# Kernel tuning notes

Measured on AMD Instinct MI355X. Metric: run time of the kernel, lower is better.

## Reference

```python
import jax, jax.numpy as jnp
import numpy as np
from jax import lax

C = 256
RED = 16
SK = 7  # spatial kernel


def setup_inputs() -> dict:
    key = jax.random.key(0)
    ks = jax.random.split(key, 12)
    b, c, h, w = 4, C, 64, 64
    cr = c // RED
    c8 = c // 8
    s = lambda fan_in: 1.0 / np.sqrt(fan_in)
    return {
        "x": jax.random.normal(ks[0], (b, c, h, w), dtype=jnp.float32),
        # channel MLP (nn.Linear weights are [out, in], no bias)
        "w1": jax.random.normal(ks[1], (cr, c), dtype=jnp.float32) * s(c),
        "w2": jax.random.normal(ks[2], (c, cr), dtype=jnp.float32) * s(cr),
        # spatial conv: [out=1, in=2, 7, 7], no bias
        "w_sp": jax.random.normal(ks[3], (1, 2, SK, SK), dtype=jnp.float32) * s(2 * SK * SK),
        # 1x1 convs (stored as [out, in]) with bias (Conv2d default bias=True)
        "wq": jax.random.normal(ks[4], (c8, c), dtype=jnp.float32) * s(c),
        "bq": jax.random.normal(ks[5], (c8,), dtype=jnp.float32) * s(c),
        "wk": jax.random.normal(ks[6], (c8, c), dtype=jnp.float32) * s(c),
        "bk": jax.random.normal(ks[7], (c8,), dtype=jnp.float32) * s(c),
        "wv": jax.random.normal(ks[8], (c, c), dtype=jnp.float32) * s(c),
        "bv": jax.random.normal(ks[9], (c,), dtype=jnp.float32) * s(c),
        "gamma": jnp.zeros((1,), dtype=jnp.float32),
    }


def reference(x, w1, w2, w_sp, wq, bq, wk, bk, wv, bv, gamma):
    b, c, h, w = x.shape
    hw = h * w

    # ---- channel attention (CBAM) ----
    avg = jnp.mean(x, axis=(2, 3))          # [b, c]
    mx = jnp.max(x, axis=(2, 3))            # [b, c]
    mlp = lambda v: jax.nn.relu(v @ w1.T) @ w2.T
    ch_att = jax.nn.sigmoid(mlp(avg) + mlp(mx))[:, :, None, None]
    x = x * ch_att

    # ---- spatial attention (CBAM) ----
    avg_s = jnp.mean(x, axis=1, keepdims=True)
    max_s = jnp.max(x, axis=1, keepdims=True)
    sp_in = jnp.concatenate([avg_s, max_s], axis=1)  # [b, 2, h, w]
    pad = SK // 2
    sp = lax.conv_general_dilated(
        sp_in, w_sp, window_strides=(1, 1), padding=[(pad, pad), (pad, pad)],
        dimension_numbers=("NCHW", "OIHW", "NCHW"))
    x = x * jax.nn.sigmoid(sp)

    # ---- non-local self-attention (single head, unscaled) ----
    q = jnp.einsum("bchw,oc->bohw", x, wq) + bq[None, :, None, None]
    k = jnp.einsum("bchw,oc->bohw", x, wk) + bk[None, :, None, None]
    v = jnp.einsum("bchw,oc->bohw", x, wv) + bv[None, :, None, None]
    q = q.reshape(b, -1, hw).transpose(0, 2, 1)   # [b, hw, c/8]
    k = k.reshape(b, -1, hw)                      # [b, c/8, hw]
    v = v.reshape(b, c, hw)                       # [b, c, hw]

    attn = jax.nn.softmax(jnp.einsum("bid,bdj->bij", q, k), axis=-1)  # [b, hw, hw]
    out = jnp.einsum("bcj,bij->bci", v, attn).reshape(b, c, h, w)

    return gamma[0] * out + x
```

## Files before the change

kernel.cpp:

```cpp
#include <hip/hip_runtime.h>
#include <math.h>

constexpr int B_  = 4;
constexpr int C_  = 256;
constexpr int HW_ = 4096;
constexpr int CR_ = 16;
constexpr int CQ_ = 32;

__device__ __forceinline__ float sigmoidf_(float x){ return 1.f/(1.f+expf(-x)); }

__device__ __forceinline__ void ch_att_inline(
    int b, int t,
    const float* __restrict__ avg, const float* __restrict__ mxv,
    const float* __restrict__ w1,  const float* __restrict__ w2,
    float* sa, float* sm, float* pa, float* pm, float* hs, float* satt){
  sa[t] = avg[b*C_+t]; sm[t] = mxv[b*C_+t];
  __syncthreads();
  int h = t >> 4, seg = t & 15;
  float qa = 0.f, qm = 0.f;
  #pragma unroll
  for (int c2 = 0; c2 < 16; c2++){
    int c = seg*16 + c2;
    float w = w1[h*C_ + c];
    qa += w*sa[c]; qm += w*sm[c];
  }
  pa[t] = qa; pm[t] = qm;
  __syncthreads();
  if (t < CR_){
    float ha = 0.f, hm = 0.f;
    #pragma unroll
    for (int s = 0; s < 16; s++){ ha += pa[t*16+s]; hm += pm[t*16+s]; }
    hs[t] = fmaxf(ha, 0.f) + fmaxf(hm, 0.f);
  }
  __syncthreads();
  float o = 0.f;
  #pragma unroll
  for (int h2 = 0; h2 < CR_; h2++) o += hs[h2]*w2[t*CR_+h2];
  satt[t] = sigmoidf_(o);
  __syncthreads();
}

__global__ void kA(const float* __restrict__ x, float* __restrict__ avg, float* __restrict__ mxv){
  int bc = blockIdx.x;
  const float4* r4 = (const float4*)(x + (size_t)bc*HW_);
  float s = 0.f, m = -INFINITY;
  for (int i = threadIdx.x; i < HW_/4; i += 256){
    float4 v = r4[i];
    s += v.x+v.y+v.z+v.w;
    m = fmaxf(m, fmaxf(fmaxf(v.x,v.y), fmaxf(v.z,v.w)));
  }
  for (int off = 32; off; off >>= 1){
    s += __shfl_down(s, off);
    m = fmaxf(m, __shfl_down(m, off));
  }
  __shared__ float ss[4], sm[4];
  int w = threadIdx.x >> 6, lane = threadIdx.x & 63;
  if (!lane){ ss[w] = s; sm[w] = m; }
  __syncthreads();
  if (!threadIdx.x){
    avg[bc] = (ss[0]+ss[1]+ss[2]+ss[3]) * (1.f/HW_);
    mxv[bc] = fmaxf(fmaxf(sm[0],sm[1]), fmaxf(sm[2],sm[3]));
  }
}

__global__ void kBC(const float* __restrict__ x,
                    const float* __restrict__ avg, const float* __restrict__ mxv,
                    const float* __restrict__ w1,  const float* __restrict__ w2,
                    float* __restrict__ avgs, float* __restrict__ maxs){
  int b = blockIdx.x >> 6, r = blockIdx.x & 63, t = threadIdx.x;
  __shared__ float sa[C_], sm[C_], pa[C_], pm[C_], hs[CR_], satt[C_];
  __shared__ float4 rs[16][16], rm[16][16];
  ch_att_inline(b, t, avg, mxv, w1, w2, sa, sm, pa, pm, hs, satt);

  int cg = t >> 4, q = t & 15;
  const float4* x4 = (const float4*)x;
  float4 s = {0.f,0.f,0.f,0.f};
  float4 m = {-INFINITY,-INFINITY,-INFINITY,-INFINITY};
  #pragma unroll
  for (int j = 0; j < 16; j++){
    int c = cg*16 + j;
    float a = satt[c];
    float4 v = x4[(size_t)(b*C_+c)*(HW_/4) + (r<<4) + q];
    float vx=v.x*a, vy=v.y*a, vz=v.z*a, vw=v.w*a;
    s.x+=vx; s.y+=vy; s.z+=vz; s.w+=vw;
    m.x=fmaxf(m.x,vx); m.y=fmaxf(m.y,vy); m.z=fmaxf(m.z,vz); m.w=fmaxf(m.w,vw);
  }
  rs[cg][q] = s; rm[cg][q] = m;
  __syncthreads();
  if (t < 16){
    float4 S = {0.f,0.f,0.f,0.f};
    float4 M = {-INFINITY,-INFINITY,-INFINITY,-INFINITY};
    #pragma unroll
    for (int g = 0; g < 16; g++){
      float4 a = rs[g][t], b2 = rm[g][t];
      S.x+=a.x; S.y+=a.y; S.z+=a.z; S.w+=a.w;
      M.x=fmaxf(M.x,b2.x); M.y=fmaxf(M.y,b2.y); M.z=fmaxf(M.z,b2.z); M.w=fmaxf(M.w,b2.w);
    }
    S.x*=(1.f/C_); S.y*=(1.f/C_); S.z*=(1.f/C_); S.w*=(1.f/C_);
    ((float4*)(avgs + b*HW_ + r*64))[t] = S;
    ((float4*)(maxs + b*HW_ + r*64))[t] = M;
  }
}

__global__ void kD2(const float* __restrict__ x,
                    const float* __restrict__ avg, const float* __restrict__ mxv,
                    const float* __restrict__ w1,  const float* __restrict__ w2,
                    const float* __restrict__ avgs, const float* __restrict__ maxs,
                    const float* __restrict__ wsp, float* __restrict__ out){
  int bx = blockIdx.x;
  int b = bx >> 6, rem = bx & 63, rt = rem >> 2, cp = rem & 3;
  int t = threadIdx.x;
  __shared__ float sa[C_], sm[C_], pa[C_], pm[C_], hs[CR_], satt[C_];
  __shared__ float savg[10][64], smax[10][64], ssig[4][64], swsp[98];
  if (t < 98) swsp[t] = wsp[t];
  ch_att_inline(b, t, avg, mxv, w1, w2, sa, sm, pa, pm, hs, satt);

  for (int idx = t; idx < 640; idx += 256){
    int row = idx >> 6, col = idx & 63;
    int gr = rt*4 - 3 + row;
    float s = 0.f, m = 0.f;
    if ((unsigned)gr < 64u){
      s = avgs[b*HW_ + gr*64 + col];
      m = maxs[b*HW_ + gr*64 + col];
    }
    savg[row][col] = s; smax[row][col] = m;
  }
  __syncthreads();
  int trow = t >> 6, col = t & 63;
  float acc = 0.f;
  #pragma unroll
  for (int ky = 0; ky < 7; ky++){
    #pragma unroll
    for (int kx = 0; kx < 7; kx++){
      int gx = col - 3 + kx;
      if ((unsigned)gx < 64u)
        acc += savg[trow+ky][gx]*swsp[ky*7+kx] + smax[trow+ky][gx]*swsp[49+ky*7+kx];
    }
  }
  ssig[trow][col] = sigmoidf_(acc);
  __syncthreads();
  int f4id = t & 63;
  float4 sg4 = ((const float4*)ssig)[f4id];
  int imgo = rt*64 + f4id;
  const float4* x4 = (const float4*)x;
  float4* o4 = (float4*)out;
  #pragma unroll
  for (int jj = 0; jj < 16; jj++){
    int lc = (t>>6) + jj*4;
    float a = satt[cp*64 + lc];
    size_t g = (size_t)(b*C_ + cp*64 + lc)*(HW_/4) + imgo;
    float4 v = x4[g];
    float4 rr;
    rr.x = v.x*a*sg4.x; rr.y = v.y*a*sg4.y; rr.z = v.z*a*sg4.z; rr.w = v.w*a*sg4.w;
    o4[g] = rr;
  }
}

__global__ void kE(const float* __restrict__ gamma, const float* __restrict__ x3,
                   const float* __restrict__ wq, const float* __restrict__ bq,
                   const float* __restrict__ wk, const float* __restrict__ bk,
                   const float* __restrict__ wv, const float* __restrict__ bv,
                   float* __restrict__ qb, float* __restrict__ kb, float* __restrict__ vb){
  if (gamma[0] == 0.f) return;
  int t = threadIdx.x;
  __shared__ float sx[C_*32];
  for (int bx = blockIdx.x; bx < 512; bx += gridDim.x){
    int b = bx >> 7, tile = bx & 127, p0 = tile*32;
    for (int idx = t; idx < C_*32; idx += 256){
      int c = idx >> 5, px = idx & 31;
      sx[idx] = x3[(size_t)(b*C_+c)*HW_ + p0 + px];
    }
    __syncthreads();
    for (int oi = t; oi < CQ_*32; oi += 256){
      int o = oi >> 5, px = oi & 31;
      float aq = bq[o], ak = bk[o];
      for (int c = 0; c < C_; c++){ float xv = sx[c*32+px]; aq += xv*wq[o*C_+c]; ak += xv*wk[o*C_+c]; }
      qb[(size_t)(b*CQ_+o)*HW_ + p0 + px] = aq;
      kb[(size_t)(b*CQ_+o)*HW_ + p0 + px] = ak;
    }
    for (int oi = t; oi < C_*32; oi += 256){
      int o = oi >> 5, px = oi & 31;
      float av = bv[o];
      for (int c = 0; c < C_; c++) av += sx[c*32+px]*wv[o*C_+c];
      vb[(size_t)(b*C_+o)*HW_ + p0 + px] = av;
    }
    __syncthreads();
  }
}

__global__ void kF2(const float* __restrict__ gamma, const float* __restrict__ qb,
                    const float* __restrict__ kb, const float* __restrict__ vb,
                    float* __restrict__ out){
  float g = gamma[0];
  if (g == 0.f) return;
  __shared__ float sq[CQ_];
  __shared__ float sl[HW_];
  __shared__ float red[8];
  int t = threadIdx.x;
  for (int gi = blockIdx.x; gi < B_*HW_; gi += gridDim.x){
    int b = gi >> 12, i = gi & (HW_-1);
    if (t < CQ_) sq[t] = qb[(size_t)(b*CQ_+t)*HW_ + i];
    __syncthreads();
    float lmax = -INFINITY;
    for (int j = t; j < HW_; j += 256){
      float l = 0.f;
      for (int d = 0; d < CQ_; d++) l += sq[d]*kb[(size_t)(b*CQ_+d)*HW_ + j];
      sl[j] = l; lmax = fmaxf(lmax, l);
    }
    for (int off = 32; off; off >>= 1) lmax = fmaxf(lmax, __shfl_down(lmax, off));
    if (!(t & 63)) red[t>>6] = lmax;
    __syncthreads();
    float M = fmaxf(fmaxf(red[0],red[1]), fmaxf(red[2],red[3]));
    float lsum = 0.f;
    for (int j = t; j < HW_; j += 256){ float p = expf(sl[j]-M); sl[j] = p; lsum += p; }
    for (int off = 32; off; off >>= 1) lsum += __shfl_down(lsum, off);
    if (!(t & 63)) red[4+(t>>6)] = lsum;
    __syncthreads();
    float inv = g/(red[4]+red[5]+red[6]+red[7]);
    float acc = 0.f;
    const float* vrow = vb + (size_t)(b*C_+t)*HW_;
    for (int j = 0; j < HW_; j++) acc += sl[j]*vrow[j];
    out[(size_t)(b*C_+t)*HW_ + i] += acc*inv;
    __syncthreads();
  }
}

extern "C" void kernel_launch(void* const* d_in, const int* in_sizes, int n_in,
                              void* d_out, int out_size, void* d_ws, size_t ws_size,
                              hipStream_t stream){
  const float* x   = (const float*)d_in[0];
  const float* w1  = (const float*)d_in[1];
  const float* w2  = (const float*)d_in[2];
  const float* wsp = (const float*)d_in[3];
  const float* wq  = (const float*)d_in[4];
  const float* bq  = (const float*)d_in[5];
  const float* wk  = (const float*)d_in[6];
  const float* bk  = (const float*)d_in[7];
  const float* wv  = (const float*)d_in[8];
  const float* bv  = (const float*)d_in[9];
  const float* gm  = (const float*)d_in[10];
  float* out = (float*)d_out;
  float* ws  = (float*)d_ws;

  float* avg  = ws;
  float* mxv  = avg  + B_*C_;
  float* avgs = mxv  + B_*C_;
  float* maxs = avgs + B_*HW_;
  float* qb   = maxs + B_*HW_;
  float* kb   = qb   + B_*CQ_*HW_;
  float* vb   = kb   + B_*CQ_*HW_;
  size_t need_attn = (size_t)((vb + (size_t)B_*C_*HW_) - ws) * sizeof(float);

  kA <<<B_*C_, 256, 0, stream>>>(x, avg, mxv);
  kBC<<<256,   256, 0, stream>>>(x, avg, mxv, w1, w2, avgs, maxs);
  kD2<<<256,   256, 0, stream>>>(x, avg, mxv, w1, w2, avgs, maxs, wsp, out);

  if (ws_size >= need_attn){
    kE <<<256, 256, 0, stream>>>(gm, out, wq, bq, wk, bk, wv, bv, qb, kb, vb);
    kF2<<<256, 256, 0, stream>>>(gm, qb, kb, vb, out);
  }
}
```

Measured before the change: 109.2 us.

## Fuse all stages into one persistent kernel with atomic grid barriers

Replaces the five kernel launches with one 256-block persistent kernel whose stages are separated by a software grid barrier built on an atomic counter. The channel-attention MLP is computed once per block after the first barrier instead of in two separate kernels. This removes per-launch overhead and inter-kernel gaps, but adds a memset launch and barrier spin costs, and relies on all 256 blocks being co-resident. The ws_size guard is also dropped.

```diff
diff --git a/kernel.cpp b/kernel.cpp
--- a/kernel.cpp
+++ b/kernel.cpp
@@ -6,221 +6,221 @@
 constexpr int HW_ = 4096;
 constexpr int CR_ = 16;
 constexpr int CQ_ = 32;
+constexpr int NB_ = 256;
 
 __device__ __forceinline__ float sigmoidf_(float x){ return 1.f/(1.f+expf(-x)); }
 
-__device__ __forceinline__ void ch_att_inline(
-    int b, int t,
-    const float* __restrict__ avg, const float* __restrict__ mxv,
-    const float* __restrict__ w1,  const float* __restrict__ w2,
-    float* sa, float* sm, float* pa, float* pm, float* hs, float* satt){
-  sa[t] = avg[b*C_+t]; sm[t] = mxv[b*C_+t];
+__device__ __forceinline__ void gbar(int* cnt, int gen){
   __syncthreads();
-  int h = t >> 4, seg = t & 15;
-  float qa = 0.f, qm = 0.f;
-  #pragma unroll
-  for (int c2 = 0; c2 < 16; c2++){
-    int c = seg*16 + c2;
-    float w = w1[h*C_ + c];
-    qa += w*sa[c]; qm += w*sm[c];
-  }
-  pa[t] = qa; pm[t] = qm;
-  __syncthreads();
-  if (t < CR_){
-    float ha = 0.f, hm = 0.f;
-    #pragma unroll
-    for (int s = 0; s < 16; s++){ ha += pa[t*16+s]; hm += pm[t*16+s]; }
-    hs[t] = fmaxf(ha, 0.f) + fmaxf(hm, 0.f);
-  }
-  __syncthreads();
-  float o = 0.f;
-  #pragma unroll
-  for (int h2 = 0; h2 < CR_; h2++) o += hs[h2]*w2[t*CR_+h2];
-  satt[t] = sigmoidf_(o);
+  if (threadIdx.x == 0){
+    __threadfence();
+    __hip_atomic_fetch_add(cnt, 1, __ATOMIC_RELEASE, __HIP_MEMORY_SCOPE_AGENT);
+    while (__hip_atomic_load(cnt, __ATOMIC_ACQUIRE, __HIP_MEMORY_SCOPE_AGENT) < gen*NB_)
+      __builtin_amdgcn_s_sleep(1);
+    __threadfence();
+  }
   __syncthreads();
 }
 
-__global__ void kA(const float* __restrict__ x, float* __restrict__ avg, float* __restrict__ mxv){
-  int bc = blockIdx.x;
-  const float4* r4 = (const float4*)(x + (size_t)bc*HW_);
-  float s = 0.f, m = -INFINITY;
-  for (int i = threadIdx.x; i < HW_/4; i += 256){
-    float4 v = r4[i];
-    s += v.x+v.y+v.z+v.w;
-    m = fmaxf(m, fmaxf(fmaxf(v.x,v.y), fmaxf(v.z,v.w)));
-  }
-  for (int off = 32; off; off >>= 1){
-    s += __shfl_down(s, off);
-    m = fmaxf(m, __shfl_down(m, off));
-  }
-  __shared__ float ss[4], sm[4];
-  int w = threadIdx.x >> 6, lane = threadIdx.x & 63;
-  if (!lane){ ss[w] = s; sm[w] = m; }
-  __syncthreads();
-  if (!threadIdx.x){
-    avg[bc] = (ss[0]+ss[1]+ss[2]+ss[3]) * (1.f/HW_);
-    mxv[bc] = fmaxf(fmaxf(sm[0],sm[1]), fmaxf(sm[2],sm[3]));
-  }
-}
-
-__global__ void kBC(const float* __restrict__ x,
-                    const float* __restrict__ avg, const float* __restrict__ mxv,
-                    const float* __restrict__ w1,  const float* __restrict__ w2,
-                    float* __restrict__ avgs, float* __restrict__ maxs){
-  int b = blockIdx.x >> 6, r = blockIdx.x & 63, t = threadIdx.x;
-  __shared__ float sa[C_], sm[C_], pa[C_], pm[C_], hs[CR_], satt[C_];
-  __shared__ float4 rs[16][16], rm[16][16];
-  ch_att_inline(b, t, avg, mxv, w1, w2, sa, sm, pa, pm, hs, satt);
-
-  int cg = t >> 4, q = t & 15;
-  const float4* x4 = (const float4*)x;
-  float4 s = {0.f,0.f,0.f,0.f};
-  float4 m = {-INFINITY,-INFINITY,-INFINITY,-INFINITY};
-  #pragma unroll
-  for (int j = 0; j < 16; j++){
-    int c = cg*16 + j;
-    float a = satt[c];
-    float4 v = x4[(size_t)(b*C_+c)*(HW_/4) + (r<<4) + q];
-    float vx=v.x*a, vy=v.y*a, vz=v.z*a, vw=v.w*a;
-    s.x+=vx; s.y+=vy; s.z+=vz; s.w+=vw;
-    m.x=fmaxf(m.x,vx); m.y=fmaxf(m.y,vy); m.z=fmaxf(m.z,vz); m.w=fmaxf(m.w,vw);
-  }
-  rs[cg][q] = s; rm[cg][q] = m;
-  __syncthreads();
-  if (t < 16){
-    float4 S = {0.f,0.f,0.f,0.f};
-    float4 M = {-INFINITY,-INFINITY,-INFINITY,-INFINITY};
-    #pragma unroll
-    for (int g = 0; g < 16; g++){
-      float4 a = rs[g][t], b2 = rm[g][t];
-      S.x+=a.x; S.y+=a.y; S.z+=a.z; S.w+=a.w;
-      M.x=fmaxf(M.x,b2.x); M.y=fmaxf(M.y,b2.y); M.z=fmaxf(M.z,b2.z); M.w=fmaxf(M.w,b2.w);
-    }
-    S.x*=(1.f/C_); S.y*=(1.f/C_); S.z*=(1.f/C_); S.w*=(1.f/C_);
-    ((float4*)(avgs + b*HW_ + r*64))[t] = S;
-    ((float4*)(maxs + b*HW_ + r*64))[t] = M;
-  }
-}
-
-__global__ void kD2(const float* __restrict__ x,
-                    const float* __restrict__ avg, const float* __restrict__ mxv,
-                    const float* __restrict__ w1,  const float* __restrict__ w2,
-                    const float* __restrict__ avgs, const float* __restrict__ maxs,
-                    const float* __restrict__ wsp, float* __restrict__ out){
-  int bx = blockIdx.x;
-  int b = bx >> 6, rem = bx & 63, rt = rem >> 2, cp = rem & 3;
-  int t = threadIdx.x;
-  __shared__ float sa[C_], sm[C_], pa[C_], pm[C_], hs[CR_], satt[C_];
-  __shared__ float savg[10][64], smax[10][64], ssig[4][64], swsp[98];
-  if (t < 98) swsp[t] = wsp[t];
-  ch_att_inline(b, t, avg, mxv, w1, w2, sa, sm, pa, pm, hs, satt);
-
-  for (int idx = t; idx < 640; idx += 256){
-    int row = idx >> 6, col = idx & 63;
-    int gr = rt*4 - 3 + row;
-    float s = 0.f, m = 0.f;
-    if ((unsigned)gr < 64u){
-      s = avgs[b*HW_ + gr*64 + col];
-      m = maxs[b*HW_ + gr*64 + col];
-    }
-    savg[row][col] = s; smax[row][col] = m;
-  }
-  __syncthreads();
-  int trow = t >> 6, col = t & 63;
-  float acc = 0.f;
-  #pragma unroll
-  for (int ky = 0; ky < 7; ky++){
-    #pragma unroll
-    for (int kx = 0; kx < 7; kx++){
-      int gx = col - 3 + kx;
-      if ((unsigned)gx < 64u)
-        acc += savg[trow+ky][gx]*swsp[ky*7+kx] + smax[trow+ky][gx]*swsp[49+ky*7+kx];
-    }
-  }
-  ssig[trow][col] = sigmoidf_(acc);
-  __syncthreads();
-  int f4id = t & 63;
-  float4 sg4 = ((const float4*)ssig)[f4id];
-  int imgo = rt*64 + f4id;
-  const float4* x4 = (const float4*)x;
-  float4* o4 = (float4*)out;
-  #pragma unroll
-  for (int jj = 0; jj < 16; jj++){
-    int lc = (t>>6) + jj*4;
-    float a = satt[cp*64 + lc];
-    size_t g = (size_t)(b*C_ + cp*64 + lc)*(HW_/4) + imgo;
-    float4 v = x4[g];
-    float4 rr;
-    rr.x = v.x*a*sg4.x; rr.y = v.y*a*sg4.y; rr.z = v.z*a*sg4.z; rr.w = v.w*a*sg4.w;
-    o4[g] = rr;
-  }
-}
-
-__global__ void kE(const float* __restrict__ gamma, const float* __restrict__ x3,
-                   const float* __restrict__ wq, const float* __restrict__ bq,
-                   const float* __restrict__ wk, const float* __restrict__ bk,
-                   const float* __restrict__ wv, const float* __restrict__ bv,
-                   float* __restrict__ qb, float* __restrict__ kb, float* __restrict__ vb){
-  if (gamma[0] == 0.f) return;
-  int t = threadIdx.x;
-  __shared__ float sx[C_*32];
-  for (int bx = blockIdx.x; bx < 512; bx += gridDim.x){
-    int b = bx >> 7, tile = bx & 127, p0 = tile*32;
+__global__ void __launch_bounds__(256, 1) kFused(
+    const float* __restrict__ x,
+    const float* __restrict__ w1,  const float* __restrict__ w2,
+    const float* __restrict__ wsp,
+    const float* __restrict__ wq,  const float* __restrict__ bq,
+    const float* __restrict__ wk,  const float* __restrict__ bk,
+    const float* __restrict__ wv,  const float* __restrict__ bv,
+    const float* __restrict__ gm,
+    int* cnt, float* avg, float* mxv, float* avgs, float* maxs,
+    float* qb, float* kb, float* vb, float* out){
+
+  __shared__ union {
+    struct {
+      float sa[C_], sm[C_], pa[C_], pm[C_], hs[CR_], satt[C_];
+      float4 rs[16][16], rm[16][16];
+      float savg[10][64], smax[10][64], ssig[4][64], swsp[98];
+    } p;
+    float sx[C_*32];
+    struct { float sq[CQ_], red[8], sl[HW_]; } f;
+  } S;
+
+  int t = threadIdx.x, bx = blockIdx.x;
+  int w = t >> 6, lane = t & 63;
+
+  {
+    int bc = bx*4 + w;
+    const float4* r4 = (const float4*)(x + (size_t)bc*HW_);
+    float s = 0.f, m = -INFINITY;
+    #pragma unroll
+    for (int k2 = 0; k2 < 16; k2++){
+      float4 v = r4[lane + k2*64];
+      s += v.x+v.y+v.z+v.w;
+      m = fmaxf(m, fmaxf(fmaxf(v.x,v.y), fmaxf(v.z,v.w)));
+    }
+    for (int off = 32; off; off >>= 1){
+      s += __shfl_down(s, off);
+      m = fmaxf(m, __shfl_down(m, off));
+    }
+    if (!lane){ avg[bc] = s*(1.f/HW_); mxv[bc] = m; }
+  }
+  gbar(cnt, 1);
+
+  int b = bx >> 6;
+  {
+    if (t < 98) S.p.swsp[t] = wsp[t];
+    S.p.sa[t] = avg[b*C_+t]; S.p.sm[t] = mxv[b*C_+t];
+    __syncthreads();
+    int h = t >> 4, seg = t & 15;
+    float qa = 0.f, qm = 0.f;
+    #pragma unroll
+    for (int c2 = 0; c2 < 16; c2++){
+      int c = seg*16 + c2;
+      float ww = w1[h*C_ + c];
+      qa += ww*S.p.sa[c]; qm += ww*S.p.sm[c];
+    }
+    S.p.pa[t] = qa; S.p.pm[t] = qm;
+    __syncthreads();
+    if (t < CR_){
+      float ha = 0.f, hm = 0.f;
+      #pragma unroll
+      for (int s2 = 0; s2 < 16; s2++){ ha += S.p.pa[t*16+s2]; hm += S.p.pm[t*16+s2]; }
+      S.p.hs[t] = fmaxf(ha, 0.f) + fmaxf(hm, 0.f);
+    }
+    __syncthreads();
+    float o = 0.f;
+    #pragma unroll
+    for (int h2 = 0; h2 < CR_; h2++) o += S.p.hs[h2]*w2[t*CR_+h2];
+    S.p.satt[t] = sigmoidf_(o);
+    __syncthreads();
+
+    int r = bx & 63;
+    int cg = t >> 4, q = t & 15;
+    const float4* x4 = (const float4*)x;
+    float4 s = {0.f,0.f,0.f,0.f};
+    float4 m = {-INFINITY,-INFINITY,-INFINITY,-INFINITY};
+    #pragma unroll
+    for (int j = 0; j < 16; j++){
+      int c = cg*16 + j;
+      float a = S.p.satt[c];
+      float4 v = x4[(size_t)(b*C_+c)*(HW_/4) + (r<<4) + q];
+      float vx=v.x*a, vy=v.y*a, vz=v.z*a, vw=v.w*a;
+      s.x+=vx; s.y+=vy; s.z+=vz; s.w+=vw;
+      m.x=fmaxf(m.x,vx); m.y=fmaxf(m.y,vy); m.z=fmaxf(m.z,vz); m.w=fmaxf(m.w,vw);
+    }
+    S.p.rs[cg][q] = s; S.p.rm[cg][q] = m;
+    __syncthreads();
+    if (t < 16){
+      float4 Sv = {0.f,0.f,0.f,0.f};
+      float4 Mv = {-INFINITY,-INFINITY,-INFINITY,-INFINITY};
+      #pragma unroll
+      for (int g2 = 0; g2 < 16; g2++){
+        float4 a = S.p.rs[g2][t], b2 = S.p.rm[g2][t];
+        Sv.x+=a.x; Sv.y+=a.y; Sv.z+=a.z; Sv.w+=a.w;
+        Mv.x=fmaxf(Mv.x,b2.x); Mv.y=fmaxf(Mv.y,b2.y); Mv.z=fmaxf(Mv.z,b2.z); Mv.w=fmaxf(Mv.w,b2.w);
+      }
+      Sv.x*=(1.f/C_); Sv.y*=(1.f/C_); Sv.z*=(1.f/C_); Sv.w*=(1.f/C_);
+      ((float4*)(avgs + b*HW_ + r*64))[t] = Sv;
+      ((float4*)(maxs + b*HW_ + r*64))[t] = Mv;
+    }
+  }
+  gbar(cnt, 2);
+
+  {
+    int rem = bx & 63, rt = rem >> 2, cp = rem & 3;
+    for (int idx = t; idx < 640; idx += 256){
+      int row = idx >> 6, col = idx & 63;
+      int gr = rt*4 - 3 + row;
+      float s = 0.f, m = 0.f;
+      if ((unsigned)gr < 64u){
+        s = avgs[b*HW_ + gr*64 + col];
+        m = maxs[b*HW_ + gr*64 + col];
+      }
+      S.p.savg[row][col] = s; S.p.smax[row][col] = m;
+    }
+    __syncthreads();
+    int trow = t >> 6, col = t & 63;
+    float acc = 0.f;
+    #pragma unroll
+    for (int ky = 0; ky < 7; ky++){
+      #pragma unroll
+      for (int kx = 0; kx < 7; kx++){
+        int gx = col - 3 + kx;
+        if ((unsigned)gx < 64u)
+          acc += S.p.savg[trow+ky][gx]*S.p.swsp[ky*7+kx]
+               + S.p.smax[trow+ky][gx]*S.p.swsp[49+ky*7+kx];
+      }
+    }
+    S.p.ssig[trow][col] = sigmoidf_(acc);
+    __syncthreads();
+    int f4id = t & 63;
+    float4 sg4 = ((const float4*)S.p.ssig)[f4id];
+    int imgo = rt*64 + f4id;
+    const float4* x4 = (const float4*)x;
+    float4* o4 = (float4*)out;
+    #pragma unroll
+    for (int jj = 0; jj < 16; jj++){
+      int lc = (t>>6) + jj*4;
+      float a = S.p.satt[cp*64 + lc];
+      size_t g = (size_t)(b*C_ + cp*64 + lc)*(HW_/4) + imgo;
+      float4 v = x4[g];
+      float4 rr;
+      rr.x = v.x*a*sg4.x; rr.y = v.y*a*sg4.y; rr.z = v.z*a*sg4.z; rr.w = v.w*a*sg4.w;
+      o4[g] = rr;
+    }
+  }
+
+  float g = gm[0];
+  if (g == 0.f) return;
+
+  gbar(cnt, 3);
+
+  for (int bx2 = bx; bx2 < 512; bx2 += NB_){
+    int b2 = bx2 >> 7, tile = bx2 & 127, p0 = tile*32;
     for (int idx = t; idx < C_*32; idx += 256){
       int c = idx >> 5, px = idx & 31;
-      sx[idx] = x3[(size_t)(b*C_+c)*HW_ + p0 + px];
+      S.sx[idx] = out[(size_t)(b2*C_+c)*HW_ + p0 + px];
     }
     __syncthreads();
     for (int oi = t; oi < CQ_*32; oi += 256){
       int o = oi >> 5, px = oi & 31;
       float aq = bq[o], ak = bk[o];
-      for (int c = 0; c < C_; c++){ float xv = sx[c*32+px]; aq += xv*wq[o*C_+c]; ak += xv*wk[o*C_+c]; }
-      qb[(size_t)(b*CQ_+o)*HW_ + p0 + px] = aq;
-      kb[(size_t)(b*CQ_+o)*HW_ + p0 + px] = ak;
+      for (int c = 0; c < C_; c++){ float xv = S.sx[c*32+px]; aq += xv*wq[o*C_+c]; ak += xv*wk[o*C_+c]; }
+      qb[(size_t)(b2*CQ_+o)*HW_ + p0 + px] = aq;
+      kb[(size_t)(b2*CQ_+o)*HW_ + p0 + px] = ak;
     }
     for (int oi = t; oi < C_*32; oi += 256){
       int o = oi >> 5, px = oi & 31;
       float av = bv[o];
-      for (int c = 0; c < C_; c++) av += sx[c*32+px]*wv[o*C_+c];
-      vb[(size_t)(b*C_+o)*HW_ + p0 + px] = av;
-    }
-    __syncthreads();
-  }
-}
-
-__global__ void kF2(const float* __restrict__ gamma, const float* __restrict__ qb,
-                    const float* __restrict__ kb, const float* __restrict__ vb,
-                    float* __restrict__ out){
-  float g = gamma[0];
-  if (g == 0.f) return;
-  __shared__ float sq[CQ_];
-  __shared__ float sl[HW_];
-  __shared__ float red[8];
-  int t = threadIdx.x;
-  for (int gi = blockIdx.x; gi < B_*HW_; gi += gridDim.x){
-    int b = gi >> 12, i = gi & (HW_-1);
-    if (t < CQ_) sq[t] = qb[(size_t)(b*CQ_+t)*HW_ + i];
+      for (int c = 0; c < C_; c++) av += S.sx[c*32+px]*wv[o*C_+c];
+      vb[(size_t)(b2*C_+o)*HW_ + p0 + px] = av;
+    }
+    __syncthreads();
+  }
+  gbar(cnt, 4);
+
+  for (int gi = bx; gi < B_*HW_; gi += NB_){
+    int b2 = gi >> 12, i = gi & (HW_-1);
+    if (t < CQ_) S.f.sq[t] = qb[(size_t)(b2*CQ_+t)*HW_ + i];
     __syncthreads();
     float lmax = -INFINITY;
     for (int j = t; j < HW_; j += 256){
       float l = 0.f;
-      for (int d = 0; d < CQ_; d++) l += sq[d]*kb[(size_t)(b*CQ_+d)*HW_ + j];
-      sl[j] = l; lmax = fmaxf(lmax, l);
+      for (int d = 0; d < CQ_; d++) l += S.f.sq[d]*kb[(size_t)(b2*CQ_+d)*HW_ + j];
+      S.f.sl[j] = l; lmax = fmaxf(lmax, l);
     }
     for (int off = 32; off; off >>= 1) lmax = fmaxf(lmax, __shfl_down(lmax, off));
-    if (!(t & 63)) red[t>>6] = lmax;
-    __syncthreads();
-    float M = fmaxf(fmaxf(red[0],red[1]), fmaxf(red[2],red[3]));
+    if (!(t & 63)) S.f.red[t>>6] = lmax;
+    __syncthreads();
+    float M = fmaxf(fmaxf(S.f.red[0],S.f.red[1]), fmaxf(S.f.red[2],S.f.red[3]));
     float lsum = 0.f;
-    for (int j = t; j < HW_; j += 256){ float p = expf(sl[j]-M); sl[j] = p; lsum += p; }
+    for (int j = t; j < HW_; j += 256){ float p = expf(S.f.sl[j]-M); S.f.sl[j] = p; lsum += p; }
     for (int off = 32; off; off >>= 1) lsum += __shfl_down(lsum, off);
-    if (!(t & 63)) red[4+(t>>6)] = lsum;
-    __syncthreads();
-    float inv = g/(red[4]+red[5]+red[6]+red[7]);
+    if (!(t & 63)) S.f.red[4+(t>>6)] = lsum;
+    __syncthreads();
+    float inv = g/(S.f.red[4]+S.f.red[5]+S.f.red[6]+S.f.red[7]);
     float acc = 0.f;
-    const float* vrow = vb + (size_t)(b*C_+t)*HW_;
-    for (int j = 0; j < HW_; j++) acc += sl[j]*vrow[j];
-    out[(size_t)(b*C_+t)*HW_ + i] += acc*inv;
+    const float* vrow = vb + (size_t)(b2*C_+t)*HW_;
+    for (int j = 0; j < HW_; j++) acc += S.f.sl[j]*vrow[j];
+    out[(size_t)(b2*C_+t)*HW_ + i] += acc*inv;
     __syncthreads();
   }
 }
@@ -242,21 +242,17 @@
   float* out = (float*)d_out;
   float* ws  = (float*)d_ws;
 
-  float* avg  = ws;
+  int*   cnt  = (int*)ws;
+  float* avg  = ws + 16;
   float* mxv  = avg  + B_*C_;
   float* avgs = mxv  + B_*C_;
   float* maxs = avgs + B_*HW_;
   float* qb   = maxs + B_*HW_;
   float* kb   = qb   + B_*CQ_*HW_;
   float* vb   = kb   + B_*CQ_*HW_;
-  size_t need_attn = (size_t)((vb + (size_t)B_*C_*HW_) - ws) * sizeof(float);
-
-  kA <<<B_*C_, 256, 0, stream>>>(x, avg, mxv);
-  kBC<<<256,   256, 0, stream>>>(x, avg, mxv, w1, w2, avgs, maxs);
-  kD2<<<256,   256, 0, stream>>>(x, avg, mxv, w1, w2, avgs, maxs, wsp, out);
-
-  if (ws_size >= need_attn){
-    kE <<<256, 256, 0, stream>>>(gm, out, wq, bq, wk, bk, wv, bv, qb, kb, vb);
-    kF2<<<256, 256, 0, stream>>>(gm, qb, kb, vb, out);
-  }
+  (void)in_sizes; (void)n_in; (void)out_size; (void)ws_size;
+
+  hipMemsetAsync(cnt, 0, 64, stream);
+  kFused<<<NB_, 256, 0, stream>>>(x, w1, w2, wsp, wq, bq, wk, bk, wv, bv, gm,
+                                  cnt, avg, mxv, avgs, maxs, qb, kb, vb, out);
 }
```

After: 139.1 us. 1.27x slower.
